# Kernel tuning notes

Hardware: AMD Instinct MI355X
Metric: run time of the kernel (lower is better)

The kernel has to match this reference:

```python
import jax, jax.numpy as jnp
import numpy as np

N = 50000
E = 500000
STRUCT = 128
SEM = 768
HID = 128
HEADS = 4


def setup_inputs() -> dict:
    key = jax.random.key(0)
    ks = jax.random.split(key, 16)
    rn = lambda k, s, sc=0.05: jax.random.normal(k, s, dtype=jnp.float32) * sc
    in_dim = STRUCT + SEM
    return {
        "x": rn(ks[0], (N, in_dim), 1.0),
        "edge_index": jax.random.randint(ks[1], (2, E), 0, N),
        "Wq": rn(ks[2], (STRUCT, HID)),
        "Wk": rn(ks[3], (SEM, HID)),
        "Wv": rn(ks[4], (SEM, HID)),
        "Wo": rn(ks[5], (STRUCT + HID, STRUCT)),
        "bo": jnp.zeros((STRUCT,), jnp.float32),
        "W1": rn(ks[6], (in_dim, HEADS * HID)),
        "att_src1": rn(ks[7], (HEADS, HID)),
        "att_dst1": rn(ks[8], (HEADS, HID)),
        "b1": jnp.zeros((HEADS * HID,), jnp.float32),
        "g1_w": jnp.ones((HEADS * HID,), jnp.float32),
        "g1_b": jnp.zeros((HEADS * HID,), jnp.float32),
        "g1_ms": jnp.ones((HEADS * HID,), jnp.float32),
        "W2": rn(ks[9], (HEADS * HID, HID)),
        "att_src2": rn(ks[10], (1, HID)),
        "att_dst2": rn(ks[11], (1, HID)),
        "b2": jnp.zeros((HID,), jnp.float32),
        "g2_w": jnp.ones((HID,), jnp.float32),
        "g2_b": jnp.zeros((HID,), jnp.float32),
        "g2_ms": jnp.ones((HID,), jnp.float32),
        "Wn": rn(ks[12], (HID, 2)),
        "bn": jnp.zeros((2,), jnp.float32),
    }


def gat_conv(x, src, dst, W, att_src, att_dst, bias, heads, out_c, concat):
    # PyG GATConv (self loops already appended to src/dst by caller)
    n = x.shape[0]
    h = (x @ W).reshape(n, heads, out_c)              # [N,H,C]
    a_src = (h * att_src).sum(-1)                      # [N,H]
    a_dst = (h * att_dst).sum(-1)                      # [N,H]
    alpha = jax.nn.leaky_relu(a_src[src] + a_dst[dst], 0.2)  # [Etot,H]
    amax = jax.ops.segment_max(alpha, dst, num_segments=n)
    amax = jnp.where(jnp.isfinite(amax), amax, 0.0)
    ex = jnp.exp(alpha - amax[dst])
    denom = jax.ops.segment_sum(ex, dst, num_segments=n)
    att = ex / (denom[dst] + 1e-16)                    # segment softmax over dst
    msg = h[src] * att[:, :, None]                     # [Etot,H,C]
    out = jax.ops.segment_sum(msg, dst, num_segments=n)
    out = out.reshape(n, heads * out_c) if concat else out.mean(1)
    return out + bias


def graph_norm(x, weight, bias, mean_scale, eps=1e-5):
    mean = x.mean(0, keepdims=True)
    out = x - mean * mean_scale
    var = (out * out).mean(0, keepdims=True)
    return out / jnp.sqrt(var + eps) * weight + bias


def reference(x, edge_index, Wq, Wk, Wv, Wo, bo, W1, att_src1, att_dst1, b1,
              g1_w, g1_b, g1_ms, W2, att_src2, att_dst2, b2, g2_w, g2_b, g2_ms,
              Wn, bn):
    x_struct = x[:, :STRUCT]
    x_sem = x[:, STRUCT:]
    # CrossModalFusion
    Q = x_struct @ Wq
    K = x_sem @ Wk
    V = x_sem @ Wv
    scores = (Q * K).sum(-1, keepdims=True)
    attn = jax.nn.sigmoid(scores) * V
    h0 = jnp.concatenate([x_struct, attn], axis=1) @ Wo + bo
    h = jnp.concatenate([h0, x_sem], axis=1)
    # add self loops once
    n = x.shape[0]
    loop = jnp.arange(n, dtype=edge_index.dtype)
    src = jnp.concatenate([edge_index[0], loop])
    dst = jnp.concatenate([edge_index[1], loop])
    h = gat_conv(h, src, dst, W1, att_src1, att_dst1, b1, HEADS, HID, True)
    h = jax.nn.elu(graph_norm(h, g1_w, g1_b, g1_ms))
    h = gat_conv(h, src, dst, W2, att_src2, att_dst2, b2, 1, HID, False)
    h = jax.nn.elu(graph_norm(h, g2_w, g2_b, g2_ms))
    return h @ Wn + bn
```

## Files before the change

### kernel.cpp

```cpp
#include <hip/hip_runtime.h>
#include <math.h>

#define NN 50000
#define NE 500000
#define EEDG 550000
#define SDIM 128
#define MDIM 768
#define HIDD 128
#define NHEADS 4
#define INDIM 896
#define H1D 512
#define SCAN_NB 196
#define MP 50048
#define MT 391

typedef unsigned short u16;
typedef unsigned int u32;
typedef __attribute__((ext_vector_type(8))) short short8;
typedef __attribute__((ext_vector_type(4))) float f32x4;

__device__ __forceinline__ u16 f2bf(float f) {
    union { float f; u32 u; } v; v.f = f;
    u32 r = v.u + 0x7FFFu + ((v.u >> 16) & 1u);
    return (u16)(r >> 16);
}
__device__ __forceinline__ float bf2f(u16 h) {
    union { u32 u; float f; } v; v.u = ((u32)h) << 16;
    return v.f;
}

__device__ __forceinline__ void gl_lds16(const u16* g, u16* l) {
    __builtin_amdgcn_global_load_lds(
        (const __attribute__((address_space(1))) void*)g,
        (__attribute__((address_space(3))) void*)l, 16, 0, 0);
}

__device__ __forceinline__ void edge_sd(const int* __restrict__ ei, int e, int& s, int& d) {
    if (e < NE) { s = ei[e]; d = ei[NE + e]; }
    else        { s = e - NE; d = e - NE; }
}

__global__ void fillk(float* __restrict__ p, float v, long count) {
    long i = (long)blockIdx.x * blockDim.x + threadIdx.x;
    long stride = (long)gridDim.x * blockDim.x;
    for (; i < count; i += stride) p[i] = v;
}

__global__ void fillk_i(int* __restrict__ p, int v, long count) {
    long i = (long)blockIdx.x * blockDim.x + threadIdx.x;
    long stride = (long)gridDim.x * blockDim.x;
    for (; i < count; i += stride) p[i] = v;
}

__global__ __launch_bounds__(256) void cast_pad_x(const float4* __restrict__ x4, u16* __restrict__ xb) {
    const long total = (long)MP * 224;
    long i = (long)blockIdx.x * blockDim.x + threadIdx.x;
    long stride = (long)gridDim.x * blockDim.x;
    for (; i < total; i += stride) {
        int row = (int)(i / 224);
        int c4 = (int)(i - (long)row * 224);
        float4 v = make_float4(0.f, 0.f, 0.f, 0.f);
        if (row < NN) v = x4[(size_t)row * 224 + c4];
        short4 o;
        o.x = (short)f2bf(v.x); o.y = (short)f2bf(v.y);
        o.z = (short)f2bf(v.z); o.w = (short)f2bf(v.w);
        *(short4*)(xb + (size_t)row * 896 + c4 * 4) = o;
    }
}

__global__ __launch_bounds__(256) void cast_wT(const float* __restrict__ W, u16* __restrict__ Wb, int K, int N) {
    int k = blockIdx.x * 4 + (threadIdx.x >> 6);
    int n = blockIdx.y * 64 + (threadIdx.x & 63);
    if (k < K && n < N) Wb[(size_t)n * K + k] = f2bf(W[(size_t)k * N + n]);
}

__global__ __launch_bounds__(256) void count_deg(const int* __restrict__ ei, int* __restrict__ deg) {
    int e = blockIdx.x * 256 + threadIdx.x;
    if (e >= EEDG) return;
    int d = e < NE ? ei[NE + e] : e - NE;
    atomicAdd(&deg[d], 1);
}

__global__ __launch_bounds__(256) void scan_bsum(const int* __restrict__ deg, int* __restrict__ part) {
    __shared__ int s[256];
    int t = threadIdx.x;
    int idx = blockIdx.x * 256 + t;
    s[t] = idx < NN ? deg[idx] : 0;
    __syncthreads();
    for (int off = 128; off; off >>= 1) {
        if (t < off) s[t] += s[t + off];
        __syncthreads();
    }
    if (t == 0) part[blockIdx.x] = s[0];
}

__global__ __launch_bounds__(256) void scan_part(int* __restrict__ part) {
    __shared__ int s[256];
    int t = threadIdx.x;
    int v = t < SCAN_NB ? part[t] : 0;
    s[t] = v;
    __syncthreads();
    for (int off = 1; off < 256; off <<= 1) {
        int x = t >= off ? s[t - off] : 0;
        __syncthreads();
        s[t] += x;
        __syncthreads();
    }
    if (t < SCAN_NB) part[t] = s[t] - v;
}

__global__ __launch_bounds__(256) void scan_write(const int* __restrict__ deg, const int* __restrict__ part,
                                                  int* __restrict__ rowptr) {
    __shared__ int s[256];
    int t = threadIdx.x;
    int idx = blockIdx.x * 256 + t;
    int v = idx < NN ? deg[idx] : 0;
    s[t] = v;
    __syncthreads();
    for (int off = 1; off < 256; off <<= 1) {
        int x = t >= off ? s[t - off] : 0;
        __syncthreads();
        s[t] += x;
        __syncthreads();
    }
    if (idx < NN) rowptr[idx] = part[blockIdx.x] + s[t] - v;
    if (idx == NN - 1) rowptr[NN] = EEDG;
}

__global__ __launch_bounds__(256) void fill_csr(const int* __restrict__ ei, const int* __restrict__ rowptr,
                                                int* __restrict__ cur, int* __restrict__ esrc) {
    int e = blockIdx.x * 256 + threadIdx.x;
    if (e >= EEDG) return;
    int s, d;
    edge_sd(ei, e, s, d);
    int p = rowptr[d] + atomicAdd(&cur[d], 1);
    esrc[p] = s;
}

template<int OUT_BF16>
__device__ __forceinline__ void gemm_body(
    u16* __restrict__ Asm, u16* __restrict__ Bsm,
    const u16* __restrict__ A1, int lda1, int K1,
    const u16* __restrict__ A2, int lda2, int K2,
    const u16* __restrict__ Bw,
    void* __restrict__ Cout, int ldc,
    const float* __restrict__ bias, int row0, int col0)
{
    const int tid = threadIdx.x;
    const int wave = tid >> 6, lane = tid & 63;
    const int wr = wave >> 1, wc = wave & 1;
    const int K = K1 + K2;
    const int srow = tid >> 2;
    const int skp = (tid & 3) * 8;
    const int l15 = lane & 15, l4 = lane >> 4;

    f32x4 acc[4][4];
    #pragma unroll
    for (int i = 0; i < 4; ++i)
        #pragma unroll
        for (int j = 0; j < 4; ++j)
            acc[i][j] = (f32x4){0.f, 0.f, 0.f, 0.f};

    for (int k0 = 0; k0 < K; k0 += 32) {
        const u16* Ab; int la; int kk;
        if (k0 < K1) { Ab = A1; la = lda1; kk = k0; }
        else         { Ab = A2; la = lda2; kk = k0 - K1; }
        gl_lds16(Ab + (size_t)(row0 + srow) * la + kk + skp,      Asm + srow * 32 + skp);
        gl_lds16(Ab + (size_t)(row0 + srow + 64) * la + kk + skp, Asm + (srow + 64) * 32 + skp);
        gl_lds16(Bw + (size_t)(col0 + srow) * K + k0 + skp,       Bsm + srow * 32 + skp);
        gl_lds16(Bw + (size_t)(col0 + srow + 64) * K + k0 + skp,  Bsm + (srow + 64) * 32 + skp);
        __syncthreads();
        short8 af[4], bfr[4];
        #pragma unroll
        for (int m = 0; m < 4; ++m)
            af[m] = *(const short8*)(Asm + (wr * 64 + m * 16 + l15) * 32 + l4 * 8);
        #pragma unroll
        for (int n = 0; n < 4; ++n)
            bfr[n] = *(const short8*)(Bsm + (wc * 64 + n * 16 + l15) * 32 + l4 * 8);
        #pragma unroll
        for (int m = 0; m < 4; ++m)
            #pragma unroll
            for (int n = 0; n < 4; ++n)
                acc[m][n] = __builtin_amdgcn_mfma_f32_16x16x32_bf16(af[m], bfr[n], acc[m][n], 0, 0, 0);
        __syncthreads();
    }
    #pragma unroll
    for (int m = 0; m < 4; ++m) {
        int r = row0 + wr * 64 + m * 16 + l4 * 4;
        #pragma unroll
        for (int n = 0; n < 4; ++n) {
            int c = col0 + wc * 64 + n * 16 + l15;
            float bv = bias ? bias[c] : 0.f;
            #pragma unroll
            for (int q = 0; q < 4; ++q) {
                float v = acc[m][n][q] + bv;
                if (OUT_BF16) ((u16*)Cout)[(size_t)(r + q) * ldc + c] = f2bf(v);
                else          ((float*)Cout)[(size_t)(r + q) * ldc + c] = v;
            }
        }
    }
}

template<int OUT_BF16>
__global__ __launch_bounds__(256) void gemm_mfma(
    const u16* __restrict__ A1, int lda1, int K1,
    const u16* __restrict__ A2, int lda2, int K2,
    const u16* __restrict__ Bw,
    void* __restrict__ Cout, int ldc,
    const float* __restrict__ bias)
{
    __shared__ u16 Asm[128 * 32];
    __shared__ u16 Bsm[128 * 32];
    gemm_body<OUT_BF16>(Asm, Bsm, A1, lda1, K1, A2, lda2, K2, Bw, Cout, ldc, bias,
                        blockIdx.y * 128, blockIdx.x * 128);
}

__global__ __launch_bounds__(256) void gemm_qkv(
    const u16* __restrict__ xb,
    const u16* __restrict__ wqT, const u16* __restrict__ wkT, const u16* __restrict__ wvT,
    u16* __restrict__ qb, u16* __restrict__ kb, u16* __restrict__ vb)
{
    __shared__ u16 Asm[128 * 32];
    __shared__ u16 Bsm[128 * 32];
    const u16* A; const u16* B; int K; u16* C;
    if (blockIdx.x == 0)      { A = xb;       B = wqT; K = 128; C = qb; }
    else if (blockIdx.x == 1) { A = xb + 128; B = wkT; K = 768; C = kb; }
    else                      { A = xb + 128; B = wvT; K = 768; C = vb; }
    gemm_body<1>(Asm, Bsm, A, 896, K, (const u16*)nullptr, 0, 0, B, C, 128, nullptr,
                 blockIdx.y * 128, 0);
}

__global__ __launch_bounds__(128) void node_attn_b(const u16* __restrict__ Q,
                                                   const u16* __restrict__ K,
                                                   u16* __restrict__ V)
{
    int nd = blockIdx.x;
    int t = threadIdx.x;
    size_t base = (size_t)nd * HIDD;
    float p = bf2f(Q[base + t]) * bf2f(K[base + t]);
    #pragma unroll
    for (int off = 32; off; off >>= 1) p += __shfl_down(p, off);
    __shared__ float sm[2];
    if ((t & 63) == 0) sm[t >> 6] = p;
    __syncthreads();
    float s = sm[0] + sm[1];
    float sig = 1.f / (1.f + expf(-s));
    V[base + t] = f2bf(bf2f(V[base + t]) * sig);
}

__global__ __launch_bounds__(256) void att_dots1_b(const u16* __restrict__ h1,
    const float* __restrict__ asv, const float* __restrict__ adv,
    float* __restrict__ a_src, float* __restrict__ a_dst)
{
    int nd = blockIdx.x;
    int t = threadIdx.x;
    int w = t >> 6, l = t & 63;
    const u16* hr = h1 + (size_t)nd * H1D + w * HIDD;
    const float* sv = asv + w * HIDD;
    const float* dv = adv + w * HIDD;
    float h0v = bf2f(hr[l]), h1v = bf2f(hr[l + 64]);
    float ps = h0v * sv[l] + h1v * sv[l + 64];
    float pd = h0v * dv[l] + h1v * dv[l + 64];
    #pragma unroll
    for (int off = 32; off; off >>= 1) {
        ps += __shfl_down(ps, off);
        pd += __shfl_down(pd, off);
    }
    if (l == 0) { a_src[nd * NHEADS + w] = ps; a_dst[nd * NHEADS + w] = pd; }
}

__global__ __launch_bounds__(128) void att_dots2_b(const u16* __restrict__ h2,
    const float* __restrict__ sv, const float* __restrict__ dv,
    float* __restrict__ a_src, float* __restrict__ a_dst)
{
    int nd = blockIdx.x;
    int t = threadIdx.x;
    float hv = bf2f(h2[(size_t)nd * HIDD + t]);
    float ps = hv * sv[t], pd = hv * dv[t];
    #pragma unroll
    for (int off = 32; off; off >>= 1) {
        ps += __shfl_down(ps, off);
        pd += __shfl_down(pd, off);
    }
    __shared__ float sm[4];
    if ((t & 63) == 0) { sm[t >> 6] = ps; sm[2 + (t >> 6)] = pd; }
    __syncthreads();
    if (t == 0) { a_src[nd] = sm[0] + sm[1]; a_dst[nd] = sm[2] + sm[3]; }
}

__global__ __launch_bounds__(256) void agg1_f(const int* __restrict__ rowptr, const int* __restrict__ esrc,
    const float* __restrict__ asrc, const float* __restrict__ adst,
    const u16* __restrict__ h1b, const float* __restrict__ bias, u16* __restrict__ o1b)
{
    __shared__ int   s_src[64];
    __shared__ float s_att[64 * NHEADS];
    int d = blockIdx.x;
    int t = threadIdx.x;
    int c0 = t * 2;
    int h = t >> 6;
    int eh = t & 3;
    int ee = t >> 2;
    int beg = rowptr[d], end = rowptr[d + 1];
    float ad_eh = adst[d * NHEADS + eh];
    float n0 = 0.f, n1 = 0.f, den = 0.f;
    for (int i0 = beg; i0 < end; i0 += 64) {
        int m = min(64, end - i0);
        float ex = 0.f; int s = 0;
        if (ee < m) {
            s = esrc[i0 + ee];
            float a = asrc[s * NHEADS + eh] + ad_eh;
            a = a >= 0.f ? a : 0.2f * a;
            ex = expf(a);
        }
        s_att[ee * NHEADS + eh] = ex;
        if (eh == 0) s_src[ee] = s;
        __syncthreads();
        int j = 0;
        for (; j + 1 < m; j += 2) {
            int sA = s_src[j], sB = s_src[j + 1];
            float aA = s_att[j * NHEADS + h], aB = s_att[(j + 1) * NHEADS + h];
            u32 pA = *(const u32*)(h1b + (size_t)sA * H1D + c0);
            u32 pB = *(const u32*)(h1b + (size_t)sB * H1D + c0);
            den += aA + aB;
            n0 = fmaf(bf2f((u16)pA), aA, n0);
            n1 = fmaf(bf2f((u16)(pA >> 16)), aA, n1);
            n0 = fmaf(bf2f((u16)pB), aB, n0);
            n1 = fmaf(bf2f((u16)(pB >> 16)), aB, n1);
        }
        if (j < m) {
            int sA = s_src[j];
            float aA = s_att[j * NHEADS + h];
            u32 pA = *(const u32*)(h1b + (size_t)sA * H1D + c0);
            den += aA;
            n0 = fmaf(bf2f((u16)pA), aA, n0);
            n1 = fmaf(bf2f((u16)(pA >> 16)), aA, n1);
        }
        __syncthreads();
    }
    float invd = 1.f / (den + 1e-16f);
    float a0o = n0 * invd + bias[c0];
    float a1o = n1 * invd + bias[c0 + 1];
    u32 o = (u32)f2bf(a0o) | ((u32)f2bf(a1o) << 16);
    *(u32*)(o1b + (size_t)d * H1D + c0) = o;
}

__global__ __launch_bounds__(256) void agg2_f(const int* __restrict__ rowptr, const int* __restrict__ esrc,
    const float* __restrict__ asrc, const float* __restrict__ adst,
    const u16* __restrict__ h2b, const float* __restrict__ bias, float* __restrict__ o2)
{
    int w = threadIdx.x >> 6, l = threadIdx.x & 63;
    int d = blockIdx.x * 4 + w;
    if (d >= NN) return;
    int c0 = l * 2;
    int beg = rowptr[d], end = rowptr[d + 1];
    float ad = adst[d];
    float n0 = 0.f, n1 = 0.f, den = 0.f;
    for (int i0 = beg; i0 < end; i0 += 64) {
        int m = min(64, end - i0);
        float ex = 0.f; int s = 0;
        if (l < m) {
            s = esrc[i0 + l];
            float a = asrc[s] + ad;
            a = a >= 0.f ? a : 0.2f * a;
            ex = expf(a);
        }
        int j = 0;
        for (; j + 1 < m; j += 2) {
            int sA = __shfl(s, j), sB = __shfl(s, j + 1);
            float aA = __shfl(ex, j), aB = __shfl(ex, j + 1);
            u32 pA = *(const u32*)(h2b + (size_t)sA * HIDD + c0);
            u32 pB = *(const u32*)(h2b + (size_t)sB * HIDD + c0);
            den += aA + aB;
            n0 = fmaf(bf2f((u16)pA), aA, n0);
            n1 = fmaf(bf2f((u16)(pA >> 16)), aA, n1);
            n0 = fmaf(bf2f((u16)pB), aB, n0);
            n1 = fmaf(bf2f((u16)(pB >> 16)), aB, n1);
        }
        if (j < m) {
            int sA = __shfl(s, j);
            float aA = __shfl(ex, j);
            u32 pA = *(const u32*)(h2b + (size_t)sA * HIDD + c0);
            den += aA;
            n0 = fmaf(bf2f((u16)pA), aA, n0);
            n1 = fmaf(bf2f((u16)(pA >> 16)), aA, n1);
        }
    }
    float invd = 1.f / (den + 1e-16f);
    o2[(size_t)d * HIDD + c0]     = n0 * invd + bias[c0];
    o2[(size_t)d * HIDD + c0 + 1] = n1 * invd + bias[c0 + 1];
}

__global__ void colstat_b(const u16* __restrict__ x, float* __restrict__ msum,
                          float* __restrict__ vsum, int n, int rpb)
{
    int C = blockDim.x;
    int c = threadIdx.x;
    int r0 = blockIdx.x * rpb;
    int r1 = min(n, r0 + rpb);
    float s = 0.f, s2 = 0.f;
    for (int r = r0; r < r1; ++r) {
        float v = bf2f(x[(size_t)r * C + c]);
        s += v;
        s2 += v * v;
    }
    atomicAdd(&msum[c], s);
    atomicAdd(&vsum[c], s2);
}

__global__ void apply_norm_elu_b(u16* __restrict__ x, const float* __restrict__ msum,
                                 const float* __restrict__ vsum, const float* __restrict__ ms,
                                 const float* __restrict__ w, const float* __restrict__ b,
                                 int n, int rpb)
{
    int C = blockDim.x;
    int c = threadIdx.x;
    const float invn = 1.f / (float)NN;
    float mean = msum[c] * invn;
    float sub = mean * ms[c];
    float var = vsum[c] * invn - 2.f * sub * mean + sub * sub;
    float inv = rsqrtf(var + 1e-5f);
    float wc = w[c] * inv, bc = b[c];
    int r0 = blockIdx.x * rpb;
    int r1 = min(n, r0 + rpb);
    for (int r = r0; r < r1; ++r) {
        float v = (bf2f(x[(size_t)r * C + c]) - sub) * wc + bc;
        v = v > 0.f ? v : expm1f(v);
        x[(size_t)r * C + c] = f2bf(v);
    }
}

__global__ void colstat(const float* __restrict__ x, float* __restrict__ msum,
                        float* __restrict__ vsum, int n, int rpb)
{
    int C = blockDim.x;
    int c = threadIdx.x;
    int r0 = blockIdx.x * rpb;
    int r1 = min(n, r0 + rpb);
    float s = 0.f, s2 = 0.f;
    for (int r = r0; r < r1; ++r) {
        float v = x[(size_t)r * C + c];
        s += v;
        s2 += v * v;
    }
    atomicAdd(&msum[c], s);
    atomicAdd(&vsum[c], s2);
}

__global__ __launch_bounds__(128) void norm2_proj(const float* __restrict__ o2,
    const float* __restrict__ msum, const float* __restrict__ vsum,
    const float* __restrict__ ms, const float* __restrict__ w, const float* __restrict__ b,
    const float* __restrict__ Wn, const float* __restrict__ bn, float* __restrict__ out)
{
    int nd = blockIdx.x;
    int t = threadIdx.x;
    const float invn = 1.f / (float)NN;
    float mean = msum[t] * invn;
    float sub = mean * ms[t];
    float var = vsum[t] * invn - 2.f * sub * mean + sub * sub;
    float inv = rsqrtf(var + 1e-5f);
    float v = (o2[(size_t)nd * HIDD + t] - sub) * w[t] * inv + b[t];
    v = v > 0.f ? v : expm1f(v);
    float p0 = v * Wn[t * 2], p1 = v * Wn[t * 2 + 1];
    #pragma unroll
    for (int off = 32; off; off >>= 1) {
        p0 += __shfl_down(p0, off);
        p1 += __shfl_down(p1, off);
    }
    __shared__ float sm[4];
    if ((t & 63) == 0) { sm[t >> 6] = p0; sm[2 + (t >> 6)] = p1; }
    __syncthreads();
    if (t == 0) {
        out[nd * 2 + 0] = sm[0] + sm[1] + bn[0];
        out[nd * 2 + 1] = sm[2] + sm[3] + bn[1];
    }
}

extern "C" void kernel_launch(void* const* d_in, const int* in_sizes, int n_in,
                              void* d_out, int out_size, void* d_ws, size_t ws_size,
                              hipStream_t stream)
{
    const float* x   = (const float*)d_in[0];
    const int*   ei  = (const int*)d_in[1];
    const float* Wq  = (const float*)d_in[2];
    const float* Wk  = (const float*)d_in[3];
    const float* Wv  = (const float*)d_in[4];
    const float* Wo  = (const float*)d_in[5];
    const float* bo  = (const float*)d_in[6];
    const float* W1  = (const float*)d_in[7];
    const float* as1 = (const float*)d_in[8];
    const float* ad1 = (const float*)d_in[9];
    const float* b1  = (const float*)d_in[10];
    const float* g1w = (const float*)d_in[11];
    const float* g1b = (const float*)d_in[12];
    const float* g1m = (const float*)d_in[13];
    const float* W2  = (const float*)d_in[14];
    const float* as2 = (const float*)d_in[15];
    const float* ad2 = (const float*)d_in[16];
    const float* b2  = (const float*)d_in[17];
    const float* g2w = (const float*)d_in[18];
    const float* g2b = (const float*)d_in[19];
    const float* g2m = (const float*)d_in[20];
    const float* Wn  = (const float*)d_in[21];
    const float* bn  = (const float*)d_in[22];
    float* out = (float*)d_out;

    u16* usw = (u16*)d_ws;
    size_t uo = 0;
    u16* xb  = usw + uo; uo += (size_t)MP * 896;
    u16* h1b = usw + uo; uo += (size_t)MP * 512;
    u16* qb  = usw + uo; uo += (size_t)MP * 128;
    u16* kb  = usw + uo; uo += (size_t)MP * 128;
    u16* vb  = usw + uo; uo += (size_t)MP * 128;
    u16* o1b = usw + uo; uo += (size_t)MP * 512;
    u16* wqT = usw + uo; uo += 128 * 128;
    u16* wkT = usw + uo; uo += 128 * 768;
    u16* wvT = usw + uo; uo += 128 * 768;
    u16* woT = usw + uo; uo += 128 * 256;
    u16* w1T = usw + uo; uo += 512 * 896;
    u16* w2T = usw + uo; uo += 128 * 512;
    float* fws = (float*)(usw + uo);
    size_t fo = 0;
    float* asrc = fws + fo; fo += NN * NHEADS;
    float* adst = fws + fo; fo += NN * NHEADS;
    float* msum = fws + fo; fo += 512;
    float* vsum = fws + fo; fo += 512;
    int* iws = (int*)(fws + fo);
    size_t io = 0;
    int* rowptr = iws + io; io += NN + 1;
    int* degcur = iws + io; io += NN;
    int* esrc   = iws + io; io += EEDG;
    int* spart  = iws + io; io += 256;
    float* o2  = (float*)xb;
    u16* h0b = qb;
    u16* h2b = kb;

    const int EB = (EEDG + 255) / 256;

    cast_wT<<<dim3(32, 2),   256, 0, stream>>>(Wq, wqT, 128, 128);
    cast_wT<<<dim3(192, 2),  256, 0, stream>>>(Wk, wkT, 768, 128);
    cast_wT<<<dim3(192, 2),  256, 0, stream>>>(Wv, wvT, 768, 128);
    cast_wT<<<dim3(64, 2),   256, 0, stream>>>(Wo, woT, 256, 128);
    cast_wT<<<dim3(224, 8),  256, 0, stream>>>(W1, w1T, 896, 512);
    cast_wT<<<dim3(128, 2),  256, 0, stream>>>(W2, w2T, 512, 128);
    cast_pad_x<<<8192, 256, 0, stream>>>((const float4*)x, xb);

    fillk_i<<<196, 256, 0, stream>>>(degcur, 0, NN);
    count_deg<<<EB, 256, 0, stream>>>(ei, degcur);
    scan_bsum<<<SCAN_NB, 256, 0, stream>>>(degcur, spart);
    scan_part<<<1, 256, 0, stream>>>(spart);
    scan_write<<<SCAN_NB, 256, 0, stream>>>(degcur, spart, rowptr);
    fillk_i<<<196, 256, 0, stream>>>(degcur, 0, NN);
    fill_csr<<<EB, 256, 0, stream>>>(ei, rowptr, degcur, esrc);

    gemm_qkv<<<dim3(3, MT), 256, 0, stream>>>(xb, wqT, wkT, wvT, qb, kb, vb);
    node_attn_b<<<NN, 128, 0, stream>>>(qb, kb, vb);

    gemm_mfma<1><<<dim3(1, MT), 256, 0, stream>>>(xb, 896, 128, vb, 128, 128, woT, h0b, 128, bo);

    gemm_mfma<1><<<dim3(4, MT), 256, 0, stream>>>(h0b, 128, 128, xb + 128, 896, 768, w1T, h1b, 512, nullptr);

    att_dots1_b<<<NN, 256, 0, stream>>>(h1b, as1, ad1, asrc, adst);
    agg1_f<<<NN, 256, 0, stream>>>(rowptr, esrc, asrc, adst, h1b, b1, o1b);

    fillk<<<4, 256, 0, stream>>>(msum, 0.f, 1024);
    colstat_b<<<(NN + 127) / 128, H1D, 0, stream>>>(o1b, msum, vsum, NN, 128);
    apply_norm_elu_b<<<(NN + 127) / 128, H1D, 0, stream>>>(o1b, msum, vsum, g1m, g1w, g1b, NN, 128);

    gemm_mfma<1><<<dim3(1, MT), 256, 0, stream>>>(o1b, 512, 512, (const u16*)nullptr, 0, 0, w2T, h2b, 128, nullptr);
    att_dots2_b<<<NN, 128, 0, stream>>>(h2b, as2, ad2, asrc, adst);
    agg2_f<<<(NN + 3) / 4, 256, 0, stream>>>(rowptr, esrc, asrc, adst, h2b, b2, o2);

    fillk<<<4, 256, 0, stream>>>(msum, 0.f, 1024);
    colstat<<<(NN + 127) / 128, HIDD, 0, stream>>>(o2, msum, vsum, NN, 128);
    norm2_proj<<<NN, 128, 0, stream>>>(o2, msum, vsum, g2m, g2w, g2b, Wn, bn, out);
}
```

Measured before the change: 649.0 us.

## Share A tiles across two weight matrices in dual-output MFMA GEMM and unroll aggregation

After: 733.2 us. +13.0%, slower.

```diff
diff --git a/kernel.cpp b/kernel.cpp
--- a/kernel.cpp
+++ b/kernel.cpp
@@ -215,19 +215,82 @@
                         blockIdx.y * 128, blockIdx.x * 128);
 }
 
-__global__ __launch_bounds__(256) void gemm_qkv(
-    const u16* __restrict__ xb,
-    const u16* __restrict__ wqT, const u16* __restrict__ wkT, const u16* __restrict__ wvT,
-    u16* __restrict__ qb, u16* __restrict__ kb, u16* __restrict__ vb)
+__global__ __launch_bounds__(256) void gemm_dual(
+    const u16* __restrict__ A1, int lda1, int K1,
+    const u16* __restrict__ A2, int lda2, int K2,
+    const u16* __restrict__ B0, const u16* __restrict__ B1,
+    u16* __restrict__ C0, u16* __restrict__ C1, int ldc)
 {
     __shared__ u16 Asm[128 * 32];
-    __shared__ u16 Bsm[128 * 32];
-    const u16* A; const u16* B; int K; u16* C;
-    if (blockIdx.x == 0)      { A = xb;       B = wqT; K = 128; C = qb; }
-    else if (blockIdx.x == 1) { A = xb + 128; B = wkT; K = 768; C = kb; }
-    else                      { A = xb + 128; B = wvT; K = 768; C = vb; }
-    gemm_body<1>(Asm, Bsm, A, 896, K, (const u16*)nullptr, 0, 0, B, C, 128, nullptr,
-                 blockIdx.y * 128, 0);
+    __shared__ u16 B0sm[128 * 32];
+    __shared__ u16 B1sm[128 * 32];
+    const int tid = threadIdx.x;
+    const int wave = tid >> 6, lane = tid & 63;
+    const int wr = wave >> 1, wc = wave & 1;
+    const int row0 = blockIdx.y * 128;
+    const int K = K1 + K2;
+    const int l15 = lane & 15, l4 = lane >> 4;
+    size_t badv = (size_t)blockIdx.x * 256 * K;
+    size_t cadv = (size_t)blockIdx.x * 256;
+    B0 += badv; B1 += badv;
+    C0 += cadv; C1 += cadv;
+    const int r0s = tid >> 1;
+    const int ca = tid, cb = tid + 256;
+    const int ra = ca >> 2, ka = (ca & 3) * 8;
+    const int rb = cb >> 2, kb_ = (cb & 3) * 8;
+    (void)r0s;
+
+    f32x4 acc0[4][4], acc1[4][4];
+    #pragma unroll
+    for (int i = 0; i < 4; ++i)
+        #pragma unroll
+        for (int j = 0; j < 4; ++j) {
+            acc0[i][j] = (f32x4){0.f, 0.f, 0.f, 0.f};
+            acc1[i][j] = (f32x4){0.f, 0.f, 0.f, 0.f};
+        }
+
+    for (int k0 = 0; k0 < K; k0 += 32) {
+        const u16* Ab; int la; int kk;
+        if (k0 < K1) { Ab = A1; la = lda1; kk = k0; }
+        else         { Ab = A2; la = lda2; kk = k0 - K1; }
+        gl_lds16(Ab + (size_t)(row0 + ra) * la + kk + ka,  Asm + ra * 32 + ka);
+        gl_lds16(Ab + (size_t)(row0 + rb) * la + kk + kb_, Asm + rb * 32 + kb_);
+        gl_lds16(B0 + (size_t)ra * K + k0 + ka,  B0sm + ra * 32 + ka);
+        gl_lds16(B0 + (size_t)rb * K + k0 + kb_, B0sm + rb * 32 + kb_);
+        gl_lds16(B1 + (size_t)ra * K + k0 + ka,  B1sm + ra * 32 + ka);
+        gl_lds16(B1 + (size_t)rb * K + k0 + kb_, B1sm + rb * 32 + kb_);
+        __syncthreads();
+        short8 af[4], b0f[4], b1f[4];
+        #pragma unroll
+        for (int m = 0; m < 4; ++m)
+            af[m] = *(const short8*)(Asm + (wr * 64 + m * 16 + l15) * 32 + l4 * 8);
+        #pragma unroll
+        for (int n = 0; n < 4; ++n) {
+            b0f[n] = *(const short8*)(B0sm + (wc * 64 + n * 16 + l15) * 32 + l4 * 8);
+            b1f[n] = *(const short8*)(B1sm + (wc * 64 + n * 16 + l15) * 32 + l4 * 8);
+        }
+        #pragma unroll
+        for (int m = 0; m < 4; ++m)
+            #pragma unroll
+            for (int n = 0; n < 4; ++n) {
+                acc0[m][n] = __builtin_amdgcn_mfma_f32_16x16x32_bf16(af[m], b0f[n], acc0[m][n], 0, 0, 0);
+                acc1[m][n] = __builtin_amdgcn_mfma_f32_16x16x32_bf16(af[m], b1f[n], acc1[m][n], 0, 0, 0);
+            }
+        __syncthreads();
+    }
+    #pragma unroll
+    for (int m = 0; m < 4; ++m) {
+        int r = row0 + wr * 64 + m * 16 + l4 * 4;
+        #pragma unroll
+        for (int n = 0; n < 4; ++n) {
+            int c = wc * 64 + n * 16 + l15;
+            #pragma unroll
+            for (int q = 0; q < 4; ++q) {
+                C0[(size_t)(r + q) * ldc + c] = f2bf(acc0[m][n][q]);
+                C1[(size_t)(r + q) * ldc + c] = f2bf(acc1[m][n][q]);
+            }
+        }
+    }
 }
 
 __global__ __launch_bounds__(128) void node_attn_b(const u16* __restrict__ Q,
@@ -316,18 +379,25 @@
         if (eh == 0) s_src[ee] = s;
         __syncthreads();
         int j = 0;
-        for (; j + 1 < m; j += 2) {
-            int sA = s_src[j], sB = s_src[j + 1];
-            float aA = s_att[j * NHEADS + h], aB = s_att[(j + 1) * NHEADS + h];
+        for (; j + 3 < m; j += 4) {
+            int sA = s_src[j], sB = s_src[j + 1], sC = s_src[j + 2], sD = s_src[j + 3];
+            float aA = s_att[j * NHEADS + h],       aB = s_att[(j + 1) * NHEADS + h];
+            float aC = s_att[(j + 2) * NHEADS + h], aD = s_att[(j + 3) * NHEADS + h];
             u32 pA = *(const u32*)(h1b + (size_t)sA * H1D + c0);
             u32 pB = *(const u32*)(h1b + (size_t)sB * H1D + c0);
-            den += aA + aB;
+            u32 pC = *(const u32*)(h1b + (size_t)sC * H1D + c0);
+            u32 pD = *(const u32*)(h1b + (size_t)sD * H1D + c0);
+            den += (aA + aB) + (aC + aD);
             n0 = fmaf(bf2f((u16)pA), aA, n0);
             n1 = fmaf(bf2f((u16)(pA >> 16)), aA, n1);
             n0 = fmaf(bf2f((u16)pB), aB, n0);
             n1 = fmaf(bf2f((u16)(pB >> 16)), aB, n1);
-        }
-        if (j < m) {
+            n0 = fmaf(bf2f((u16)pC), aC, n0);
+            n1 = fmaf(bf2f((u16)(pC >> 16)), aC, n1);
+            n0 = fmaf(bf2f((u16)pD), aD, n0);
+            n1 = fmaf(bf2f((u16)(pD >> 16)), aD, n1);
+        }
+        for (; j < m; ++j) {
             int sA = s_src[j];
             float aA = s_att[j * NHEADS + h];
             u32 pA = *(const u32*)(h1b + (size_t)sA * H1D + c0);
@@ -365,18 +435,24 @@
             ex = expf(a);
         }
         int j = 0;
-        for (; j + 1 < m; j += 2) {
-            int sA = __shfl(s, j), sB = __shfl(s, j + 1);
-            float aA = __shfl(ex, j), aB = __shfl(ex, j + 1);
+        for (; j + 3 < m; j += 4) {
+            int sA = __shfl(s, j), sB = __shfl(s, j + 1), sC = __shfl(s, j + 2), sD = __shfl(s, j + 3);
+            float aA = __shfl(ex, j), aB = __shfl(ex, j + 1), aC = __shfl(ex, j + 2), aD = __shfl(ex, j + 3);
             u32 pA = *(const u32*)(h2b + (size_t)sA * HIDD + c0);
             u32 pB = *(const u32*)(h2b + (size_t)sB * HIDD + c0);
-            den += aA + aB;
+            u32 pC = *(const u32*)(h2b + (size_t)sC * HIDD + c0);
+            u32 pD = *(const u32*)(h2b + (size_t)sD * HIDD + c0);
+            den += (aA + aB) + (aC + aD);
             n0 = fmaf(bf2f((u16)pA), aA, n0);
             n1 = fmaf(bf2f((u16)(pA >> 16)), aA, n1);
             n0 = fmaf(bf2f((u16)pB), aB, n0);
             n1 = fmaf(bf2f((u16)(pB >> 16)), aB, n1);
-        }
-        if (j < m) {
+            n0 = fmaf(bf2f((u16)pC), aC, n0);
+            n1 = fmaf(bf2f((u16)(pC >> 16)), aC, n1);
+            n0 = fmaf(bf2f((u16)pD), aD, n0);
+            n1 = fmaf(bf2f((u16)(pD >> 16)), aD, n1);
+        }
+        for (; j < m; ++j) {
             int sA = __shfl(s, j);
             float aA = __shfl(ex, j);
             u32 pA = *(const u32*)(h2b + (size_t)sA * HIDD + c0);
@@ -527,9 +603,10 @@
     int* iws = (int*)(fws + fo);
     size_t io = 0;
     int* rowptr = iws + io; io += NN + 1;
-    int* degcur = iws + io; io += NN;
+    int* degcur = iws + io; io += 2 * NN;
     int* esrc   = iws + io; io += EEDG;
     int* spart  = iws + io; io += 256;
+    int* cur    = degcur + NN;
     float* o2  = (float*)xb;
     u16* h0b = qb;
     u16* h2b = kb;
@@ -544,20 +621,22 @@
     cast_wT<<<dim3(128, 2),  256, 0, stream>>>(W2, w2T, 512, 128);
     cast_pad_x<<<8192, 256, 0, stream>>>((const float4*)x, xb);
 
-    fillk_i<<<196, 256, 0, stream>>>(degcur, 0, NN);
+    fillk_i<<<392, 256, 0, stream>>>(degcur, 0, 2 * NN);
     count_deg<<<EB, 256, 0, stream>>>(ei, degcur);
     scan_bsum<<<SCAN_NB, 256, 0, stream>>>(degcur, spart);
     scan_part<<<1, 256, 0, stream>>>(spart);
     scan_write<<<SCAN_NB, 256, 0, stream>>>(degcur, spart, rowptr);
-    fillk_i<<<196, 256, 0, stream>>>(degcur, 0, NN);
-    fill_csr<<<EB, 256, 0, stream>>>(ei, rowptr, degcur, esrc);
-
-    gemm_qkv<<<dim3(3, MT), 256, 0, stream>>>(xb, wqT, wkT, wvT, qb, kb, vb);
+    fill_csr<<<EB, 256, 0, stream>>>(ei, rowptr, cur, esrc);
+
+    gemm_mfma<1><<<dim3(1, MT), 256, 0, stream>>>(xb, 896, 128, (const u16*)nullptr, 0, 0, wqT, qb, 128, nullptr);
+    gemm_dual<<<dim3(1, MT), 256, 0, stream>>>(xb + 128, 896, 768, (const u16*)nullptr, 0, 0,
+                                               wkT, wvT, kb, vb, 128);
     node_attn_b<<<NN, 128, 0, stream>>>(qb, kb, vb);
 
     gemm_mfma<1><<<dim3(1, MT), 256, 0, stream>>>(xb, 896, 128, vb, 128, 128, woT, h0b, 128, bo);
 
-    gemm_mfma<1><<<dim3(4, MT), 256, 0, stream>>>(h0b, 128, 128, xb + 128, 896, 768, w1T, h1b, 512, nullptr);
+    gemm_dual<<<dim3(2, MT), 256, 0, stream>>>(h0b, 128, 128, xb + 128, 896, 768,
+                                               w1T, w1T + (size_t)128 * 896, h1b, h1b + 128, 512);
 
     att_dots1_b<<<NN, 256, 0, stream>>>(h1b, as1, ad1, asrc, adst);
     agg1_f<<<NN, 256, 0, stream>>>(rowptr, esrc, asrc, adst, h1b, b1, o1b);
```

## Precompute per-edge attention exponentials in a separate kernel before aggregation

Applied to the files above, without the earlier changes.

New measurement: 652.8 us. No clear change (+0.6%).

```diff
diff --git a/kernel.cpp b/kernel.cpp
--- a/kernel.cpp
+++ b/kernel.cpp
@@ -128,13 +128,39 @@
 }
 
 __global__ __launch_bounds__(256) void fill_csr(const int* __restrict__ ei, const int* __restrict__ rowptr,
-                                                int* __restrict__ cur, int* __restrict__ esrc) {
+                                                int* __restrict__ cur, int* __restrict__ esrc,
+                                                int* __restrict__ edst) {
     int e = blockIdx.x * 256 + threadIdx.x;
     if (e >= EEDG) return;
     int s, d;
     edge_sd(ei, e, s, d);
     int p = rowptr[d] + atomicAdd(&cur[d], 1);
     esrc[p] = s;
+    edst[p] = d;
+}
+
+template<int H>
+__global__ __launch_bounds__(256) void edge_exp(const int* __restrict__ esrc, const int* __restrict__ edst,
+    const float* __restrict__ asrc, const float* __restrict__ adst, float* __restrict__ exf)
+{
+    int i = blockIdx.x * 256 + threadIdx.x;
+    if (i >= EEDG) return;
+    int s = esrc[i], d = edst[i];
+    if (H == 4) {
+        float4 as = *(const float4*)(asrc + s * 4);
+        float4 ad = *(const float4*)(adst + d * 4);
+        float4 o;
+        float a;
+        a = as.x + ad.x; a = a >= 0.f ? a : 0.2f * a; o.x = expf(a);
+        a = as.y + ad.y; a = a >= 0.f ? a : 0.2f * a; o.y = expf(a);
+        a = as.z + ad.z; a = a >= 0.f ? a : 0.2f * a; o.z = expf(a);
+        a = as.w + ad.w; a = a >= 0.f ? a : 0.2f * a; o.w = expf(a);
+        *(float4*)(exf + (size_t)i * 4) = o;
+    } else {
+        float a = asrc[s] + adst[d];
+        a = a >= 0.f ? a : 0.2f * a;
+        exf[i] = expf(a);
+    }
 }
 
 template<int OUT_BF16>
@@ -289,53 +315,41 @@
 }
 
 __global__ __launch_bounds__(256) void agg1_f(const int* __restrict__ rowptr, const int* __restrict__ esrc,
-    const float* __restrict__ asrc, const float* __restrict__ adst,
+    const float* __restrict__ exf,
     const u16* __restrict__ h1b, const float* __restrict__ bias, u16* __restrict__ o1b)
 {
-    __shared__ int   s_src[64];
-    __shared__ float s_att[64 * NHEADS];
     int d = blockIdx.x;
     int t = threadIdx.x;
     int c0 = t * 2;
     int h = t >> 6;
-    int eh = t & 3;
-    int ee = t >> 2;
     int beg = rowptr[d], end = rowptr[d + 1];
-    float ad_eh = adst[d * NHEADS + eh];
     float n0 = 0.f, n1 = 0.f, den = 0.f;
-    for (int i0 = beg; i0 < end; i0 += 64) {
-        int m = min(64, end - i0);
-        float ex = 0.f; int s = 0;
-        if (ee < m) {
-            s = esrc[i0 + ee];
-            float a = asrc[s * NHEADS + eh] + ad_eh;
-            a = a >= 0.f ? a : 0.2f * a;
-            ex = expf(a);
-        }
-        s_att[ee * NHEADS + eh] = ex;
-        if (eh == 0) s_src[ee] = s;
-        __syncthreads();
-        int j = 0;
-        for (; j + 1 < m; j += 2) {
-            int sA = s_src[j], sB = s_src[j + 1];
-            float aA = s_att[j * NHEADS + h], aB = s_att[(j + 1) * NHEADS + h];
-            u32 pA = *(const u32*)(h1b + (size_t)sA * H1D + c0);
-            u32 pB = *(const u32*)(h1b + (size_t)sB * H1D + c0);
-            den += aA + aB;
-            n0 = fmaf(bf2f((u16)pA), aA, n0);
-            n1 = fmaf(bf2f((u16)(pA >> 16)), aA, n1);
-            n0 = fmaf(bf2f((u16)pB), aB, n0);
-            n1 = fmaf(bf2f((u16)(pB >> 16)), aB, n1);
-        }
-        if (j < m) {
-            int sA = s_src[j];
-            float aA = s_att[j * NHEADS + h];
-            u32 pA = *(const u32*)(h1b + (size_t)sA * H1D + c0);
-            den += aA;
-            n0 = fmaf(bf2f((u16)pA), aA, n0);
-            n1 = fmaf(bf2f((u16)(pA >> 16)), aA, n1);
-        }
-        __syncthreads();
+    int i = beg;
+    for (; i + 3 < end; i += 4) {
+        int sA = esrc[i], sB = esrc[i + 1], sC = esrc[i + 2], sD = esrc[i + 3];
+        float aA = exf[(size_t)i * 4 + h],       aB = exf[(size_t)(i + 1) * 4 + h];
+        float aC = exf[(size_t)(i + 2) * 4 + h], aD = exf[(size_t)(i + 3) * 4 + h];
+        u32 pA = *(const u32*)(h1b + (size_t)sA * H1D + c0);
+        u32 pB = *(const u32*)(h1b + (size_t)sB * H1D + c0);
+        u32 pC = *(const u32*)(h1b + (size_t)sC * H1D + c0);
+        u32 pD = *(const u32*)(h1b + (size_t)sD * H1D + c0);
+        den += (aA + aB) + (aC + aD);
+        n0 = fmaf(bf2f((u16)pA), aA, n0);
+        n1 = fmaf(bf2f((u16)(pA >> 16)), aA, n1);
+        n0 = fmaf(bf2f((u16)pB), aB, n0);
+        n1 = fmaf(bf2f((u16)(pB >> 16)), aB, n1);
+        n0 = fmaf(bf2f((u16)pC), aC, n0);
+        n1 = fmaf(bf2f((u16)(pC >> 16)), aC, n1);
+        n0 = fmaf(bf2f((u16)pD), aD, n0);
+        n1 = fmaf(bf2f((u16)(pD >> 16)), aD, n1);
+    }
+    for (; i < end; ++i) {
+        int sA = esrc[i];
+        float aA = exf[(size_t)i * 4 + h];
+        u32 pA = *(const u32*)(h1b + (size_t)sA * H1D + c0);
+        den += aA;
+        n0 = fmaf(bf2f((u16)pA), aA, n0);
+        n1 = fmaf(bf2f((u16)(pA >> 16)), aA, n1);
     }
     float invd = 1.f / (den + 1e-16f);
     float a0o = n0 * invd + bias[c0];
@@ -345,7 +359,7 @@
 }
 
 __global__ __launch_bounds__(256) void agg2_f(const int* __restrict__ rowptr, const int* __restrict__ esrc,
-    const float* __restrict__ asrc, const float* __restrict__ adst,
+    const float* __restrict__ exf,
     const u16* __restrict__ h2b, const float* __restrict__ bias, float* __restrict__ o2)
 {
     int w = threadIdx.x >> 6, l = threadIdx.x & 63;
@@ -353,37 +367,32 @@
     if (d >= NN) return;
     int c0 = l * 2;
     int beg = rowptr[d], end = rowptr[d + 1];
-    float ad = adst[d];
     float n0 = 0.f, n1 = 0.f, den = 0.f;
-    for (int i0 = beg; i0 < end; i0 += 64) {
-        int m = min(64, end - i0);
-        float ex = 0.f; int s = 0;
-        if (l < m) {
-            s = esrc[i0 + l];
-            float a = asrc[s] + ad;
-            a = a >= 0.f ? a : 0.2f * a;
-            ex = expf(a);
-        }
-        int j = 0;
-        for (; j + 1 < m; j += 2) {
-            int sA = __shfl(s, j), sB = __shfl(s, j + 1);
-            float aA = __shfl(ex, j), aB = __shfl(ex, j + 1);
-            u32 pA = *(const u32*)(h2b + (size_t)sA * HIDD + c0);
-            u32 pB = *(const u32*)(h2b + (size_t)sB * HIDD + c0);
-            den += aA + aB;
-            n0 = fmaf(bf2f((u16)pA), aA, n0);
-            n1 = fmaf(bf2f((u16)(pA >> 16)), aA, n1);
-            n0 = fmaf(bf2f((u16)pB), aB, n0);
-            n1 = fmaf(bf2f((u16)(pB >> 16)), aB, n1);
-        }
-        if (j < m) {
-            int sA = __shfl(s, j);
-            float aA = __shfl(ex, j);
-            u32 pA = *(const u32*)(h2b + (size_t)sA * HIDD + c0);
-            den += aA;
-            n0 = fmaf(bf2f((u16)pA), aA, n0);
-            n1 = fmaf(bf2f((u16)(pA >> 16)), aA, n1);
-        }
+    int i = beg;
+    for (; i + 3 < end; i += 4) {
+        int sA = esrc[i], sB = esrc[i + 1], sC = esrc[i + 2], sD = esrc[i + 3];
+        float aA = exf[i], aB = exf[i + 1], aC = exf[i + 2], aD = exf[i + 3];
+        u32 pA = *(const u32*)(h2b + (size_t)sA * HIDD + c0);
+        u32 pB = *(const u32*)(h2b + (size_t)sB * HIDD + c0);
+        u32 pC = *(const u32*)(h2b + (size_t)sC * HIDD + c0);
+        u32 pD = *(const u32*)(h2b + (size_t)sD * HIDD + c0);
+        den += (aA + aB) + (aC + aD);
+        n0 = fmaf(bf2f((u16)pA), aA, n0);
+        n1 = fmaf(bf2f((u16)(pA >> 16)), aA, n1);
+        n0 = fmaf(bf2f((u16)pB), aB, n0);
+        n1 = fmaf(bf2f((u16)(pB >> 16)), aB, n1);
+        n0 = fmaf(bf2f((u16)pC), aC, n0);
+        n1 = fmaf(bf2f((u16)(pC >> 16)), aC, n1);
+        n0 = fmaf(bf2f((u16)pD), aD, n0);
+        n1 = fmaf(bf2f((u16)(pD >> 16)), aD, n1);
+    }
+    for (; i < end; ++i) {
+        int sA = esrc[i];
+        float aA = exf[i];
+        u32 pA = *(const u32*)(h2b + (size_t)sA * HIDD + c0);
+        den += aA;
+        n0 = fmaf(bf2f((u16)pA), aA, n0);
+        n1 = fmaf(bf2f((u16)(pA >> 16)), aA, n1);
     }
     float invd = 1.f / (den + 1e-16f);
     o2[(size_t)d * HIDD + c0]     = n0 * invd + bias[c0];
@@ -522,14 +531,17 @@
     size_t fo = 0;
     float* asrc = fws + fo; fo += NN * NHEADS;
     float* adst = fws + fo; fo += NN * NHEADS;
+    float* exf  = fws + fo; fo += (size_t)EEDG * NHEADS;
     float* msum = fws + fo; fo += 512;
     float* vsum = fws + fo; fo += 512;
     int* iws = (int*)(fws + fo);
     size_t io = 0;
     int* rowptr = iws + io; io += NN + 1;
-    int* degcur = iws + io; io += NN;
+    int* degcur = iws + io; io += 2 * NN;
     int* esrc   = iws + io; io += EEDG;
+    int* edst   = iws + io; io += EEDG;
     int* spart  = iws + io; io += 256;
+    int* cur    = degcur + NN;
     float* o2  = (float*)xb;
     u16* h0b = qb;
     u16* h2b = kb;
@@ -544,13 +556,12 @@
     cast_wT<<<dim3(128, 2),  256, 0, stream>>>(W2, w2T, 512, 128);
     cast_pad_x<<<8192, 256, 0, stream>>>((const float4*)x, xb);
 
-    fillk_i<<<196, 256, 0, stream>>>(degcur, 0, NN);
+    fillk_i<<<392, 256, 0, stream>>>(degcur, 0, 2 * NN);
     count_deg<<<EB, 256, 0, stream>>>(ei, degcur);
     scan_bsum<<<SCAN_NB, 256, 0, stream>>>(degcur, spart);
     scan_part<<<1, 256, 0, stream>>>(spart);
     scan_write<<<SCAN_NB, 256, 0, stream>>>(degcur, spart, rowptr);
-    fillk_i<<<196, 256, 0, stream>>>(degcur, 0, NN);
-    fill_csr<<<EB, 256, 0, stream>>>(ei, rowptr, degcur, esrc);
+    fill_csr<<<EB, 256, 0, stream>>>(ei, rowptr, cur, esrc, edst);
 
     gemm_qkv<<<dim3(3, MT), 256, 0, stream>>>(xb, wqT, wkT, wvT, qb, kb, vb);
     node_attn_b<<<NN, 128, 0, stream>>>(qb, kb, vb);
@@ -560,7 +571,8 @@
     gemm_mfma<1><<<dim3(4, MT), 256, 0, stream>>>(h0b, 128, 128, xb + 128, 896, 768, w1T, h1b, 512, nullptr);
 
     att_dots1_b<<<NN, 256, 0, stream>>>(h1b, as1, ad1, asrc, adst);
-    agg1_f<<<NN, 256, 0, stream>>>(rowptr, esrc, asrc, adst, h1b, b1, o1b);
+    edge_exp<NHEADS><<<EB, 256, 0, stream>>>(esrc, edst, asrc, adst, exf);
+    agg1_f<<<NN, 256, 0, stream>>>(rowptr, esrc, exf, h1b, b1, o1b);
 
     fillk<<<4, 256, 0, stream>>>(msum, 0.f, 1024);
     colstat_b<<<(NN + 127) / 128, H1D, 0, stream>>>(o1b, msum, vsum, NN, 128);
@@ -568,7 +580,8 @@
 
     gemm_mfma<1><<<dim3(1, MT), 256, 0, stream>>>(o1b, 512, 512, (const u16*)nullptr, 0, 0, w2T, h2b, 128, nullptr);
     att_dots2_b<<<NN, 128, 0, stream>>>(h2b, as2, ad2, asrc, adst);
-    agg2_f<<<(NN + 3) / 4, 256, 0, stream>>>(rowptr, esrc, asrc, adst, h2b, b2, o2);
+    edge_exp<1><<<EB, 256, 0, stream>>>(esrc, edst, asrc, adst, exf);
+    agg2_f<<<(NN + 3) / 4, 256, 0, stream>>>(rowptr, esrc, exf, h2b, b2, o2);
 
     fillk<<<4, 256, 0, stream>>>(msum, 0.f, 1024);
     colstat<<<(NN + 127) / 128, HIDD, 0, stream>>>(o2, msum, vsum, NN, 128);
```
